# Performance work log

Measured on AMD Instinct MI355X. Metric: run time of the kernel, lower is better.

## Reference

```python
import jax, jax.numpy as jnp
import numpy as np
from jax import lax

B, CIN, COUT, H, W = 8, 128, 128, 128, 128
HID = COUT // 2  # expansion 0.5
K = 3            # kernel size
PAD = 1


def silu(v):
    return v * jax.nn.sigmoid(v)


def base_conv1x1(x, w, s, b):
    # 1x1 conv (no bias) + folded-BN affine (scale s, bias b) + SiLU
    y = jnp.einsum('bchw,oc->bohw', x, w)
    return silu(y * s[None, :, None, None] + b[None, :, None, None])


def bilinear_gather(img, py, px):
    Hin, Win = img.shape[1], img.shape[2]
    y0 = jnp.floor(py)
    x0 = jnp.floor(px)
    wy = py - y0
    wx = px - x0

    def corner(yc, xc):
        valid = (yc >= 0) & (yc <= Hin - 1) & (xc >= 0) & (xc <= Win - 1)
        yi = jnp.clip(yc, 0, Hin - 1).astype(jnp.int32)
        xi = jnp.clip(xc, 0, Win - 1).astype(jnp.int32)
        v = img[:, yi, xi]  # [C, Kk, H, W]
        return v * valid[None].astype(img.dtype)

    v00 = corner(y0, x0)
    v01 = corner(y0, x0 + 1)
    v10 = corner(y0 + 1, x0)
    v11 = corner(y0 + 1, x0 + 1)
    wy = wy[None]
    wx = wx[None]
    return (v00 * (1 - wy) * (1 - wx) + v01 * (1 - wy) * wx
            + v10 * wy * (1 - wx) + v11 * wy * wx)


def deform_conv_depthwise(x, off_w, off_b, dw):
    # x: [B, C, H, W]; off_w: [2*K*K, C, 3, 3]; dw: [C, K, K] (depthwise, groups=C)
    b, c, h, w = x.shape
    off = lax.conv_general_dilated(
        x, off_w, window_strides=(1, 1), padding=((PAD, PAD), (PAD, PAD)),
        dimension_numbers=('NCHW', 'OIHW', 'NCHW'))
    off = off + off_b[None, :, None, None]
    off = off.reshape(b, K * K, 2, h, w)  # torchvision: (dy, dx) per tap
    dy, dx = off[:, :, 0], off[:, :, 1]   # [B, 9, H, W]

    ky = jnp.repeat(jnp.arange(K, dtype=x.dtype), K)  # [9]
    kx = jnp.tile(jnp.arange(K, dtype=x.dtype), K)
    yy = jnp.arange(h, dtype=x.dtype)[None, :, None]  # [1, H, 1]
    xx = jnp.arange(w, dtype=x.dtype)[None, None, :]
    py = yy + ky[:, None, None] - PAD  # [9, H, W]
    px = xx + kx[:, None, None] - PAD
    py = py[None] + dy  # [B, 9, H, W]
    px = px[None] + dx

    sampled = jax.vmap(bilinear_gather)(x, py, px)  # [B, C, 9, H, W]
    return jnp.einsum('bckhw,ck->bchw', sampled, dw.reshape(c, K * K))


def setup_inputs() -> dict:
    key = jax.random.key(0)
    ks = jax.random.split(key, 12)
    f = jnp.float32
    inp = {
        'x': jax.random.normal(ks[0], (B, CIN, H, W), f),
        'w1': jax.random.normal(ks[1], (HID, CIN), f) * 0.05,
        's1': jnp.ones((HID,), f), 'b1': jnp.zeros((HID,), f),
        'w2': jax.random.normal(ks[2], (HID, CIN), f) * 0.05,
        's2': jnp.ones((HID,), f), 'b2': jnp.zeros((HID,), f),
        'w3': jax.random.normal(ks[3], (COUT, 2 * HID), f) * 0.05,
        's3': jnp.ones((COUT,), f), 'b3': jnp.zeros((COUT,), f),
        'off_w': jax.random.normal(ks[4], (2 * K * K, HID, K, K), f) * 0.01,
        'off_b': jnp.zeros((2 * K * K,), f),
        'dw': jax.random.normal(ks[5], (HID, K, K), f) * 0.1,
    }
    return inp


def reference(x, w1, s1, b1, w2, s2, b2, w3, s3, b3, off_w, off_b, dw):
    x1 = base_conv1x1(x, w1, s1, b1)          # [B, HID, H, W]
    x2 = base_conv1x1(x, w2, s2, b2)          # [B, HID, H, W]
    x1 = deform_conv_depthwise(x1, off_w, off_b, dw)
    xc = jnp.concatenate([x1, x2], axis=1)    # [B, 2*HID, H, W]
    return base_conv1x1(xc, w3, s3, b3)       # [B, COUT, H, W]
```

## Files before the change

### kernel.cpp

```cpp
#include <hip/hip_runtime.h>

typedef unsigned short u16;
typedef unsigned int   u32;
typedef unsigned char  u8;

#define BB    8
#define CINC  128
#define HIDC  64
#define COUTC 128
#define HH    128
#define WWD   128
#define HWN   16384
#define NPOS  (BB*HWN)

typedef __attribute__((ext_vector_type(8))) short bf16x8;
typedef __attribute__((ext_vector_type(4))) float f32x4;

__device__ __forceinline__ float b2f(u16 u){
    union { u32 i; float f; } v; v.i = ((u32)u) << 16; return v.f;
}
__device__ __forceinline__ u16 f2b(float f){
    union { float f; u32 i; } v; v.f = f;
    u32 i = v.i;
    i += 0x7fffu + ((i >> 16) & 1u);
    return (u16)(i >> 16);
}
__device__ __forceinline__ float blo(u32 u){
    union { u32 i; float f; } v; v.i = u << 16; return v.f;
}
__device__ __forceinline__ float bhi(u32 u){
    union { u32 i; float f; } v; v.i = u & 0xFFFF0000u; return v.f;
}
__device__ __forceinline__ float silu(float y){
    return y / (1.f + __expf(-y));
}

template<bool ISB>
__device__ __forceinline__ float ldp(const void* p, int i){
    if (ISB) return b2f(((const u16*)p)[i]);
    return ((const float*)p)[i];
}

template<bool ISB>
__device__ __forceinline__ void k0_body(
    const void* w1, const void* s1, const void* b1,
    const void* w2, const void* s2, const void* b2,
    const void* w3, const void* s3, const void* b3,
    const void* offw, const void* offb, const void* dw,
    u16* __restrict__ wbc, u16* __restrict__ wb3,
    float* __restrict__ bfc, float* __restrict__ bf3,
    u16* __restrict__ wA, float* __restrict__ ob32, float* __restrict__ dwfT)
{
    int t = blockIdx.x*256 + threadIdx.x;
    if (t < 8192){
        wbc[t] = f2b(ldp<ISB>(w1,t) * ldp<ISB>(s1,t>>7));
    } else if (t < 16384){
        int u = t - 8192;
        wbc[t] = f2b(ldp<ISB>(w2,u) * ldp<ISB>(s2,u>>7));
    }
    if (t < 16384){
        wb3[t] = f2b(ldp<ISB>(w3,t) * ldp<ISB>(s3,t>>7));
    }
    if (t < 18432){
        int set  = t / 9216, rem = t % 9216;
        int tap  = rem / 1024; int rem2 = rem % 1024;
        int chunk= rem2 >> 9;  int rem3 = rem2 & 511;
        int lane = rem3 >> 3;  int jp   = rem3 & 7;
        int jg   = set*16 + (lane & 15);
        int c    = chunk*32 + (lane>>4)*8 + jp;
        float v  = (jg < 18) ? ldp<ISB>(offw, (jg*HIDC + c)*9 + tap) : 0.f;
        wA[t] = f2b(v);
    }
    if (t < HIDC)  bfc[t]      = ldp<ISB>(b1,t);
    if (t >= HIDC && t < 2*HIDC) bfc[t] = ldp<ISB>(b2,t-HIDC);
    if (t < COUTC) bf3[t] = ldp<ISB>(b3,t);
    if (t < 32)    ob32[t] = (t < 18) ? ldp<ISB>(offb,t) : 0.f;
    if (t < HIDC*9){
        int c = t / 9, k = t % 9;
        dwfT[k*HIDC + c] = ldp<ISB>(dw,t);
    }
}

__global__ __launch_bounds__(256) void k0_prep(
    const void* w1, const void* s1, const void* b1,
    const void* w2, const void* s2, const void* b2,
    const void* w3, const void* s3, const void* b3,
    const void* offw, const void* offb, const void* dw,
    u16* wbc, u16* wb3, float* bfc, float* bf3,
    u16* wA, float* ob32, float* dwfT)
{
    bool isb = (((const u32*)s1)[0] == 0x3F803F80u);
    if (isb) k0_body<true >(w1,s1,b1,w2,s2,b2,w3,s3,b3,offw,offb,dw,wbc,wb3,bfc,bf3,wA,ob32,dwfT);
    else     k0_body<false>(w1,s1,b1,w2,s2,b2,w3,s3,b3,offw,offb,dw,wbc,wb3,bfc,bf3,wA,ob32,dwfT);
}

template<bool ISB>
__device__ __forceinline__ void k1_body(const void* __restrict__ xv,
    const u16* __restrict__ wbc, const float* __restrict__ bfc,
    u16* __restrict__ x1, u16* __restrict__ x2, u8* __restrict__ ldsb)
{
    const int lane = threadIdx.x & 63;
    const int n    = lane & 15;
    const int quad = lane >> 4;
    u8* mylds = ldsb + (threadIdx.x>>6)*4096;
    bf16x8 w[8][4];
    #pragma unroll
    for (int mt = 0; mt < 8; ++mt)
        #pragma unroll
        for (int t = 0; t < 4; ++t)
            w[mt][t] = *(const bf16x8*)(wbc + (mt*16 + n)*CINC + t*32 + quad*8);
    float4 bias[8];
    #pragma unroll
    for (int mt = 0; mt < 8; ++mt)
        bias[mt] = *(const float4*)(bfc + mt*16 + quad*4);

    const int wv = blockIdx.x*4 + (threadIdx.x >> 6);
    const int posbase = wv*16;
    const int bidx = posbase >> 14;
    const int hwb  = posbase & (HWN-1);
    f32x4 acc[8];
    #pragma unroll
    for (int mt = 0; mt < 8; ++mt) acc[mt] = (f32x4){0.f,0.f,0.f,0.f};
    #pragma unroll
    for (int t = 0; t < 4; ++t){
        bf16x8 bfr;
        if (ISB){
            const u16* xb = (const u16*)xv + (size_t)bidx*CINC*HWN + hwb + n;
            #pragma unroll
            for (int j = 0; j < 8; ++j)
                bfr[j] = (short)xb[(size_t)(t*32 + quad*8 + j)*HWN];
        } else {
            const float* xb = (const float*)xv + (size_t)bidx*CINC*HWN + hwb + n;
            #pragma unroll
            for (int j = 0; j < 8; ++j)
                bfr[j] = (short)f2b(xb[(size_t)(t*32 + quad*8 + j)*HWN]);
        }
        #pragma unroll
        for (int mt = 0; mt < 8; ++mt)
            acc[mt] = __builtin_amdgcn_mfma_f32_16x16x32_bf16(w[mt][t], bfr, acc[mt], 0,0,0);
    }
    #pragma unroll
    for (int mt = 0; mt < 8; ++mt){
        u32 lo = (u32)f2b(silu(acc[mt][0]+bias[mt].x)) | ((u32)f2b(silu(acc[mt][1]+bias[mt].y))<<16);
        u32 hi = (u32)f2b(silu(acc[mt][2]+bias[mt].z)) | ((u32)f2b(silu(acc[mt][3]+bias[mt].w))<<16);
        int chb = mt*32 + quad*8;
        int sw  = chb ^ ((n&3)<<5);
        *(uint2*)(mylds + n*256 + sw) = make_uint2(lo,hi);
    }
    #pragma unroll
    for (int i = 0; i < 2; ++i){
        int pp = i*8 + (lane>>3);
        int cb = (lane&7)*16;
        int sw = cb ^ ((pp&3)<<5);
        uint4 v1 = *(const uint4*)(mylds + pp*256 + sw);
        uint4 v2 = *(const uint4*)(mylds + pp*256 + 128 + sw);
        *(uint4*)((char*)x1 + (size_t)(posbase+pp)*128 + cb) = v1;
        *(uint4*)((char*)x2 + (size_t)(posbase+pp)*128 + cb) = v2;
    }
}

__global__ __launch_bounds__(256, 2) void k1_mfma(const void* x, const u32* s1probe,
    const u16* wbc, const float* bfc, u16* x1, u16* x2)
{
    __shared__ u8 ldsb[4*4096];
    bool isb = (s1probe[0] == 0x3F803F80u);
    if (isb) k1_body<true >(x, wbc, bfc, x1, x2, ldsb);
    else     k1_body<false>(x, wbc, bfc, x1, x2, ldsb);
}

__global__ __launch_bounds__(256) void k2_mfma(const u16* __restrict__ x1,
    const u16* __restrict__ wA, const float* __restrict__ ob32,
    float* __restrict__ offT)
{
    const int lane = threadIdx.x & 63;
    const int n    = lane & 15;
    const int quad = lane >> 4;
    const int tile = blockIdx.x*4 + (threadIdx.x >> 6);
    const int posbase = tile*16;
    const int b   = posbase >> 14;
    const int hw  = posbase & (HWN-1);
    const int y   = hw >> 7;
    const int x0  = hw & (WWD-1);
    const int xb  = x0 + n - 1;
    const u16* bbase = x1 + (size_t)b*HWN*HIDC;

    f32x4 acc0 = (f32x4){0.f,0.f,0.f,0.f};
    f32x4 acc1 = (f32x4){0.f,0.f,0.f,0.f};

    #pragma unroll
    for (int ky = 0; ky < 3; ++ky){
        int ys = y + ky - 1;
        if ((unsigned)ys >= HH) continue;
        const u16* rowp = bbase + (size_t)ys*WWD*HIDC;
        #pragma unroll
        for (int kx = 0; kx < 3; ++kx){
            int  xs  = xb + kx;
            int  xcl = min(max(xs, 0), WWD-1);
            bool vx  = ((unsigned)xs < WWD);
            const int tap = ky*3 + kx;
            #pragma unroll
            for (int ch = 0; ch < 2; ++ch){
                bf16x8 bfr = *(const bf16x8*)(rowp + xcl*HIDC + ch*32 + quad*8);
                if (!vx) bfr = (bf16x8){0,0,0,0,0,0,0,0};
                bf16x8 a0 = *(const bf16x8*)(wA + ((0*9 + tap)*2 + ch)*512 + lane*8);
                bf16x8 a1 = *(const bf16x8*)(wA + ((1*9 + tap)*2 + ch)*512 + lane*8);
                acc0 = __builtin_amdgcn_mfma_f32_16x16x32_bf16(a0, bfr, acc0, 0,0,0);
                acc1 = __builtin_amdgcn_mfma_f32_16x16x32_bf16(a1, bfr, acc1, 0,0,0);
            }
        }
    }
    #pragma unroll
    for (int r = 0; r < 4; ++r){
        int j0 = quad*4 + r;
        offT[(size_t)j0*NPOS + posbase + n] = acc0[r] + ob32[j0];
        int j1 = 16 + quad*4 + r;
        if (j1 < 18)
            offT[(size_t)j1*NPOS + posbase + n] = acc1[r] + ob32[j1];
    }
}

__global__ __launch_bounds__(256, 2) void k3b_gather(const u16* __restrict__ x1,
    const float* __restrict__ offT, const float* __restrict__ dwfT,
    u16* __restrict__ x1d)
{
    __shared__ float s_dwf[576];
    __shared__ __align__(16) u8 s_meta[16*208];

    const int tid  = threadIdx.x;
    if (tid < 144)
        *(float4*)(s_dwf + tid*4) = *(const float4*)(dwfT + tid*4);

    const int lane = tid & 63;
    const int gw   = blockIdx.x*4 + (tid >> 6);
    const int posw = gw << 2;
    const int p    = lane >> 4;
    const int li   = lane & 15;
    const int pos  = posw + p;
    const int slot = (tid >> 4) * 208;

    if (li < 9){
        const int k = li;
        int hw = pos & (HWN-1);
        int y  = hw >> 7, x = hw & (WWD-1);
        float dy = offT[(size_t)(2*k  )*NPOS + pos];
        float dx = offT[(size_t)(2*k+1)*NPOS + pos];
        float py = (float)(y + k/3 - 1) + dy;
        float px = (float)(x + k%3 - 1) + dx;
        float fy = floorf(py), fx = floorf(px);
        float wy = py - fy,    wx = px - fx;
        int y0 = (int)fy, x0i = (int)fx;
        float vy0 = ((unsigned)y0      < HH)  ? 1.f : 0.f;
        float vy1 = ((unsigned)(y0+1)  < HH)  ? 1.f : 0.f;
        float vx0 = ((unsigned)x0i     < WWD) ? 1.f : 0.f;
        float vx1 = ((unsigned)(x0i+1) < WWD) ? 1.f : 0.f;
        int yc0 = min(max(y0,   0), HH-1),  yc1 = min(max(y0+1, 0), HH-1);
        int xc0 = min(max(x0i,  0), WWD-1), xc1 = min(max(x0i+1, 0), WWD-1);
        float wy1 = 1.f - wy, wx1 = 1.f - wx;
        float4 w4;
        w4.x = wy1*wx1*vy0*vx0;
        w4.y = wy1*wx *vy0*vx1;
        w4.z = wy *wx1*vy1*vx0;
        w4.w = wy *wx *vy1*vx1;
        int o0 = (yc0*WWD + xc0)*HIDC;
        int sx = (xc1 != xc0) ? 1 : 0;
        int sy = (yc1 != yc0) ? 1 : 0;
        *(int*)   (s_meta + slot + 4*k)       = o0 | (sx<<20) | (sy<<21);
        *(float4*)(s_meta + slot + 48 + 16*k) = w4;
    }
    __syncthreads();

    const int b = posw >> 14;
    const u32* xb32 = (const u32*)(x1 + (size_t)b*HWN*HIDC) + li*2;

    float acc0 = 0.f, acc1 = 0.f, acc2 = 0.f, acc3 = 0.f;
    #pragma unroll
    for (int k = 0; k < 9; ++k){
        const int    pk  = *(const int*)   (s_meta + slot + 4*k);
        const float4 f   = *(const float4*)(s_meta + slot + 48 + 16*k);
        const float4 dwf = *(const float4*)(s_dwf + k*HIDC + li*4);
        const int o0  = (pk & 0xFFFFF) >> 1;
        const int dxs = (pk & (1<<20)) ? (HIDC>>1)       : 0;
        const int dys = (pk & (1<<21)) ? ((WWD*HIDC)>>1) : 0;
        const uint2 q00 = *(const uint2*)(xb32 + o0);
        const uint2 q01 = *(const uint2*)(xb32 + o0 + dxs);
        const uint2 q10 = *(const uint2*)(xb32 + o0 + dys);
        const uint2 q11 = *(const uint2*)(xb32 + o0 + dys + dxs);

        float s0 = blo(q00.x)*f.x + blo(q01.x)*f.y + blo(q10.x)*f.z + blo(q11.x)*f.w;
        float s1 = bhi(q00.x)*f.x + bhi(q01.x)*f.y + bhi(q10.x)*f.z + bhi(q11.x)*f.w;
        float s2 = blo(q00.y)*f.x + blo(q01.y)*f.y + blo(q10.y)*f.z + blo(q11.y)*f.w;
        float s3 = bhi(q00.y)*f.x + bhi(q01.y)*f.y + bhi(q10.y)*f.z + bhi(q11.y)*f.w;
        acc0 += s0*dwf.x;
        acc1 += s1*dwf.y;
        acc2 += s2*dwf.z;
        acc3 += s3*dwf.w;
    }

    const u32 r0 = ((u32)f2b(acc1) << 16) | (u32)f2b(acc0);
    const u32 r1 = ((u32)f2b(acc3) << 16) | (u32)f2b(acc2);
    uint2* outp = (uint2*)((u32*)x1d + (size_t)pos*(HIDC/2) + li*2);
    *outp = make_uint2(r0, r1);
}

template<bool ISB>
__device__ __forceinline__ void k4_body(const u16* __restrict__ x1d,
    const u16* __restrict__ x2,
    const u16* __restrict__ wb3, const float* __restrict__ bf3,
    void* __restrict__ out)
{
    const int lane = threadIdx.x & 63;
    const int n    = lane & 15;
    const int quad = lane >> 4;
    bf16x8 w[8][4];
    #pragma unroll
    for (int mt = 0; mt < 8; ++mt)
        #pragma unroll
        for (int t = 0; t < 4; ++t)
            w[mt][t] = *(const bf16x8*)(wb3 + (mt*16 + n)*CINC + t*32 + quad*8);
    float4 bias[8];
    #pragma unroll
    for (int mt = 0; mt < 8; ++mt)
        bias[mt] = *(const float4*)(bf3 + mt*16 + quad*4);

    const int wv = blockIdx.x*4 + (threadIdx.x >> 6);
    const int posbase = wv*16;
    const int bidx = posbase >> 14;
    const int hwb  = posbase & (HWN-1);
    f32x4 acc[8];
    #pragma unroll
    for (int mt = 0; mt < 8; ++mt) acc[mt] = (f32x4){0.f,0.f,0.f,0.f};
    const size_t rowb = (size_t)(posbase + n)*HIDC;
    #pragma unroll
    for (int t = 0; t < 4; ++t){
        const u16* src = (t < 2) ? x1d : x2;
        bf16x8 bfr = *(const bf16x8*)(src + rowb + (t&1)*32 + quad*8);
        #pragma unroll
        for (int mt = 0; mt < 8; ++mt)
            acc[mt] = __builtin_amdgcn_mfma_f32_16x16x32_bf16(w[mt][t], bfr, acc[mt], 0,0,0);
    }
    u16*   ob16 = (u16*)  out + (size_t)bidx*COUTC*HWN + hwb + n;
    float* obf  = (float*)out + (size_t)bidx*COUTC*HWN + hwb + n;
    #pragma unroll
    for (int mt = 0; mt < 8; ++mt){
        #pragma unroll
        for (int r = 0; r < 4; ++r){
            const int o = mt*16 + quad*4 + r;
            const float v = silu(acc[mt][r] + bias[mt][r]);
            if (ISB) ob16[(size_t)o*HWN] = f2b(v);
            else     obf [(size_t)o*HWN] = v;
        }
    }
}

__global__ __launch_bounds__(256, 2) void k4_mfma(const u16* x1d, const u16* x2,
    const u32* s1probe, const u16* wb3, const float* bf3, void* out)
{
    bool isb = (s1probe[0] == 0x3F803F80u);
    if (isb) k4_body<true >(x1d, x2, wb3, bf3, out);
    else     k4_body<false>(x1d, x2, wb3, bf3, out);
}

extern "C" void kernel_launch(void* const* d_in, const int* in_sizes, int n_in,
                              void* d_out, int out_size, void* d_ws, size_t ws_size,
                              hipStream_t stream)
{
    const void* x    = d_in[0];
    const void* w1   = d_in[1];
    const void* s1   = d_in[2];
    const void* b1   = d_in[3];
    const void* w2   = d_in[4];
    const void* s2   = d_in[5];
    const void* b2   = d_in[6];
    const void* w3   = d_in[7];
    const void* s3   = d_in[8];
    const void* b3   = d_in[9];
    const void* offw = d_in[10];
    const void* offb = d_in[11];
    const void* dw   = d_in[12];

    char* ws = (char*)d_ws;
    u16*   x1    = (u16*)  (ws + 0);
    u16*   x2    = (u16*)  (ws + 16777216);
    u16*   x1d   = (u16*)  (ws + 33554432);
    float* offT  = (float*)(ws + 50331648);
    u16*   wbc   = (u16*)  (ws + 59768832);
    u16*   wb3   = (u16*)  (ws + 59801600);
    u16*   wA    = (u16*)  (ws + 59834368);
    float* dwfT  = (float*)(ws + 59871232);
    float* bfc   = (float*)(ws + 59873536);
    float* bf3   = (float*)(ws + 59874048);
    float* ob32  = (float*)(ws + 59874560);

    k0_prep<<<72, 256, 0, stream>>>(w1,s1,b1, w2,s2,b2, w3,s3,b3, offw,offb,dw,
                                    wbc, wb3, bfc, bf3, wA, ob32, dwfT);
    k1_mfma  <<<2048, 256, 0, stream>>>(x, (const u32*)s1, wbc, bfc, x1, x2);
    k2_mfma  <<<2048, 256, 0, stream>>>(x1, wA, ob32, offT);
    k3b_gather<<<NPOS/16, 256, 0, stream>>>(x1, offT, dwfT, x1d);
    k4_mfma  <<<2048, 256, 0, stream>>>(x1d, x2, (const u32*)s1, wb3, bf3, d_out);
}
```

Baseline: 266.9 us.

## Stage input tile in LDS and split output channels across waves in 1x1 convs

The first 1x1 conv kernel now has each block cooperatively load a 64-position by 128-channel input tile with wide vector loads. It packs channel pairs into LDS, so the old strided per-element global gathers go away. Each wave then computes 32 output channels over all 64 positions instead of 128 channels over 16 positions, which cuts per-wave weight registers. The final 1x1 conv uses the same wave/channel split. Outputs are written directly without the LDS transpose, which may make the x1/x2 stores less coalesced.

```diff
diff --git a/kernel.cpp b/kernel.cpp
--- a/kernel.cpp
+++ b/kernel.cpp
@@ -97,75 +97,99 @@
 template<bool ISB>
 __device__ __forceinline__ void k1_body(const void* __restrict__ xv,
     const u16* __restrict__ wbc, const float* __restrict__ bfc,
-    u16* __restrict__ x1, u16* __restrict__ x2, u8* __restrict__ ldsb)
-{
+    u16* __restrict__ x1, u16* __restrict__ x2, u8* __restrict__ sx8)
+{
+    const int posb = blockIdx.x*64;
+    const int bidx = posb >> 14;
+    const int hwb  = posb & (HWN-1);
+
+    {
+        const int R  = threadIdx.x >> 2;
+        const int qq = threadIdx.x & 3;
+        u32* dst = (u32*)(sx8 + R*272 + qq*64);
+        if (ISB){
+            const u16* r0 = (const u16*)xv + (size_t)bidx*CINC*HWN + (size_t)(2*R)*HWN + hwb + qq*16;
+            const u16* r1 = r0 + HWN;
+            uint4 a0 = *(const uint4*)(r0);
+            uint4 a1 = *(const uint4*)(r0 + 8);
+            uint4 c0 = *(const uint4*)(r1);
+            uint4 c1 = *(const uint4*)(r1 + 8);
+            u32 A[8] = {a0.x,a0.y,a0.z,a0.w,a1.x,a1.y,a1.z,a1.w};
+            u32 C[8] = {c0.x,c0.y,c0.z,c0.w,c1.x,c1.y,c1.z,c1.w};
+            #pragma unroll
+            for (int k = 0; k < 8; ++k){
+                dst[2*k]   = (A[k] & 0xFFFFu) | (C[k] << 16);
+                dst[2*k+1] = (A[k] >> 16)     | (C[k] & 0xFFFF0000u);
+            }
+        } else {
+            const float* r0 = (const float*)xv + (size_t)bidx*CINC*HWN + (size_t)(2*R)*HWN + hwb + qq*16;
+            const float* r1 = r0 + HWN;
+            #pragma unroll
+            for (int k = 0; k < 8; ++k){
+                float2 f0 = *(const float2*)(r0 + 2*k);
+                float2 f1 = *(const float2*)(r1 + 2*k);
+                dst[2*k]   = (u32)f2b(f0.x) | ((u32)f2b(f1.x) << 16);
+                dst[2*k+1] = (u32)f2b(f0.y) | ((u32)f2b(f1.y) << 16);
+            }
+        }
+    }
+    __syncthreads();
+
+    const int w    = threadIdx.x >> 6;
     const int lane = threadIdx.x & 63;
     const int n    = lane & 15;
     const int quad = lane >> 4;
-    u8* mylds = ldsb + (threadIdx.x>>6)*4096;
-    bf16x8 w[8][4];
-    #pragma unroll
-    for (int mt = 0; mt < 8; ++mt)
+
+    bf16x8 wf[2][4];
+    #pragma unroll
+    for (int m = 0; m < 2; ++m)
         #pragma unroll
         for (int t = 0; t < 4; ++t)
-            w[mt][t] = *(const bf16x8*)(wbc + (mt*16 + n)*CINC + t*32 + quad*8);
-    float4 bias[8];
-    #pragma unroll
-    for (int mt = 0; mt < 8; ++mt)
-        bias[mt] = *(const float4*)(bfc + mt*16 + quad*4);
-
-    const int wv = blockIdx.x*4 + (threadIdx.x >> 6);
-    const int posbase = wv*16;
-    const int bidx = posbase >> 14;
-    const int hwb  = posbase & (HWN-1);
-    f32x4 acc[8];
-    #pragma unroll
-    for (int mt = 0; mt < 8; ++mt) acc[mt] = (f32x4){0.f,0.f,0.f,0.f};
+            wf[m][t] = *(const bf16x8*)(wbc + (size_t)(w*32 + m*16 + n)*CINC + t*32 + quad*8);
+
+    f32x4 acc[2][4];
+    #pragma unroll
+    for (int m = 0; m < 2; ++m)
+        #pragma unroll
+        for (int s = 0; s < 4; ++s) acc[m][s] = (f32x4){0.f,0.f,0.f,0.f};
+
     #pragma unroll
     for (int t = 0; t < 4; ++t){
-        bf16x8 bfr;
-        if (ISB){
-            const u16* xb = (const u16*)xv + (size_t)bidx*CINC*HWN + hwb + n;
+        #pragma unroll
+        for (int sub = 0; sub < 4; ++sub){
+            union { u32 u[4]; bf16x8 v; } bb;
             #pragma unroll
-            for (int j = 0; j < 8; ++j)
-                bfr[j] = (short)xb[(size_t)(t*32 + quad*8 + j)*HWN];
-        } else {
-            const float* xb = (const float*)xv + (size_t)bidx*CINC*HWN + hwb + n;
-            #pragma unroll
-            for (int j = 0; j < 8; ++j)
-                bfr[j] = (short)f2b(xb[(size_t)(t*32 + quad*8 + j)*HWN]);
-        }
-        #pragma unroll
-        for (int mt = 0; mt < 8; ++mt)
-            acc[mt] = __builtin_amdgcn_mfma_f32_16x16x32_bf16(w[mt][t], bfr, acc[mt], 0,0,0);
-    }
-    #pragma unroll
-    for (int mt = 0; mt < 8; ++mt){
-        u32 lo = (u32)f2b(silu(acc[mt][0]+bias[mt].x)) | ((u32)f2b(silu(acc[mt][1]+bias[mt].y))<<16);
-        u32 hi = (u32)f2b(silu(acc[mt][2]+bias[mt].z)) | ((u32)f2b(silu(acc[mt][3]+bias[mt].w))<<16);
-        int chb = mt*32 + quad*8;
-        int sw  = chb ^ ((n&3)<<5);
-        *(uint2*)(mylds + n*256 + sw) = make_uint2(lo,hi);
-    }
-    #pragma unroll
-    for (int i = 0; i < 2; ++i){
-        int pp = i*8 + (lane>>3);
-        int cb = (lane&7)*16;
-        int sw = cb ^ ((pp&3)<<5);
-        uint4 v1 = *(const uint4*)(mylds + pp*256 + sw);
-        uint4 v2 = *(const uint4*)(mylds + pp*256 + 128 + sw);
-        *(uint4*)((char*)x1 + (size_t)(posbase+pp)*128 + cb) = v1;
-        *(uint4*)((char*)x2 + (size_t)(posbase+pp)*128 + cb) = v2;
-    }
-}
-
-__global__ __launch_bounds__(256, 2) void k1_mfma(const void* x, const u32* s1probe,
+            for (int jp = 0; jp < 4; ++jp)
+                bb.u[jp] = *(const u32*)(sx8 + (t*16 + quad*4 + jp)*272 + (sub*16 + n)*4);
+            acc[0][sub] = __builtin_amdgcn_mfma_f32_16x16x32_bf16(wf[0][t], bb.v, acc[0][sub], 0,0,0);
+            acc[1][sub] = __builtin_amdgcn_mfma_f32_16x16x32_bf16(wf[1][t], bb.v, acc[1][sub], 0,0,0);
+        }
+    }
+
+    #pragma unroll
+    for (int m = 0; m < 2; ++m){
+        const int ob = w*32 + m*16 + quad*4;
+        float4 bi = *(const float4*)(bfc + ob);
+        u16* dbuf = (ob < 64) ? x1 : x2;
+        const int oo = ob & 63;
+        #pragma unroll
+        for (int sub = 0; sub < 4; ++sub){
+            const u32 lo = (u32)f2b(silu(acc[m][sub][0] + bi.x))
+                         | ((u32)f2b(silu(acc[m][sub][1] + bi.y)) << 16);
+            const u32 hi = (u32)f2b(silu(acc[m][sub][2] + bi.z))
+                         | ((u32)f2b(silu(acc[m][sub][3] + bi.w)) << 16);
+            *(uint2*)(dbuf + (size_t)(posb + sub*16 + n)*HIDC + oo) = make_uint2(lo, hi);
+        }
+    }
+}
+
+__global__ __launch_bounds__(256) void k1_mfma(const void* x, const u32* s1probe,
     const u16* wbc, const float* bfc, u16* x1, u16* x2)
 {
-    __shared__ u8 ldsb[4*4096];
+    __shared__ __align__(16) u8 sx8[64*272];
     bool isb = (s1probe[0] == 0x3F803F80u);
-    if (isb) k1_body<true >(x, wbc, bfc, x1, x2, ldsb);
-    else     k1_body<false>(x, wbc, bfc, x1, x2, ldsb);
+    if (isb) k1_body<true >(x, wbc, bfc, x1, x2, sx8);
+    else     k1_body<false>(x, wbc, bfc, x1, x2, sx8);
 }
 
 __global__ __launch_bounds__(256) void k2_mfma(const u16* __restrict__ x1,
@@ -308,51 +332,59 @@
     const u16* __restrict__ wb3, const float* __restrict__ bf3,
     void* __restrict__ out)
 {
+    const int posb = blockIdx.x*64;
+    const int bidx = posb >> 14;
+    const int hwb  = posb & (HWN-1);
+    const int w    = threadIdx.x >> 6;
     const int lane = threadIdx.x & 63;
     const int n    = lane & 15;
     const int quad = lane >> 4;
-    bf16x8 w[8][4];
-    #pragma unroll
-    for (int mt = 0; mt < 8; ++mt)
+
+    bf16x8 wf[2][4];
+    #pragma unroll
+    for (int m = 0; m < 2; ++m)
         #pragma unroll
         for (int t = 0; t < 4; ++t)
-            w[mt][t] = *(const bf16x8*)(wb3 + (mt*16 + n)*CINC + t*32 + quad*8);
-    float4 bias[8];
-    #pragma unroll
-    for (int mt = 0; mt < 8; ++mt)
-        bias[mt] = *(const float4*)(bf3 + mt*16 + quad*4);
-
-    const int wv = blockIdx.x*4 + (threadIdx.x >> 6);
-    const int posbase = wv*16;
-    const int bidx = posbase >> 14;
-    const int hwb  = posbase & (HWN-1);
-    f32x4 acc[8];
-    #pragma unroll
-    for (int mt = 0; mt < 8; ++mt) acc[mt] = (f32x4){0.f,0.f,0.f,0.f};
-    const size_t rowb = (size_t)(posbase + n)*HIDC;
+            wf[m][t] = *(const bf16x8*)(wb3 + (size_t)(w*32 + m*16 + n)*CINC + t*32 + quad*8);
+
+    f32x4 acc[2][4];
+    #pragma unroll
+    for (int m = 0; m < 2; ++m)
+        #pragma unroll
+        for (int s = 0; s < 4; ++s) acc[m][s] = (f32x4){0.f,0.f,0.f,0.f};
+
     #pragma unroll
     for (int t = 0; t < 4; ++t){
         const u16* src = (t < 2) ? x1d : x2;
-        bf16x8 bfr = *(const bf16x8*)(src + rowb + (t&1)*32 + quad*8);
-        #pragma unroll
-        for (int mt = 0; mt < 8; ++mt)
-            acc[mt] = __builtin_amdgcn_mfma_f32_16x16x32_bf16(w[mt][t], bfr, acc[mt], 0,0,0);
-    }
-    u16*   ob16 = (u16*)  out + (size_t)bidx*COUTC*HWN + hwb + n;
-    float* obf  = (float*)out + (size_t)bidx*COUTC*HWN + hwb + n;
-    #pragma unroll
-    for (int mt = 0; mt < 8; ++mt){
-        #pragma unroll
-        for (int r = 0; r < 4; ++r){
-            const int o = mt*16 + quad*4 + r;
-            const float v = silu(acc[mt][r] + bias[mt][r]);
-            if (ISB) ob16[(size_t)o*HWN] = f2b(v);
-            else     obf [(size_t)o*HWN] = v;
-        }
-    }
-}
-
-__global__ __launch_bounds__(256, 2) void k4_mfma(const u16* x1d, const u16* x2,
+        #pragma unroll
+        for (int sub = 0; sub < 4; ++sub){
+            bf16x8 bfr = *(const bf16x8*)(src + (size_t)(posb + sub*16 + n)*HIDC + (t&1)*32 + quad*8);
+            acc[0][sub] = __builtin_amdgcn_mfma_f32_16x16x32_bf16(wf[0][t], bfr, acc[0][sub], 0,0,0);
+            acc[1][sub] = __builtin_amdgcn_mfma_f32_16x16x32_bf16(wf[1][t], bfr, acc[1][sub], 0,0,0);
+        }
+    }
+
+    u16*   ob16 = (u16*)  out + (size_t)bidx*COUTC*HWN + hwb;
+    float* obf  = (float*)out + (size_t)bidx*COUTC*HWN + hwb;
+    #pragma unroll
+    for (int m = 0; m < 2; ++m){
+        const int ob = w*32 + m*16 + quad*4;
+        float4 bi = *(const float4*)(bf3 + ob);
+        #pragma unroll
+        for (int sub = 0; sub < 4; ++sub){
+            const int pp = sub*16 + n;
+            #pragma unroll
+            for (int r = 0; r < 4; ++r){
+                const float bv = (r==0)?bi.x:(r==1)?bi.y:(r==2)?bi.z:bi.w;
+                const float v = silu(acc[m][sub][r] + bv);
+                if (ISB) ob16[(size_t)(ob+r)*HWN + pp] = f2b(v);
+                else     obf [(size_t)(ob+r)*HWN + pp] = v;
+            }
+        }
+    }
+}
+
+__global__ __launch_bounds__(256) void k4_mfma(const u16* x1d, const u16* x2,
     const u32* s1probe, const u16* wb3, const float* bf3, void* out)
 {
     bool isb = (s1probe[0] == 0x3F803F80u);
@@ -393,8 +425,8 @@
 
     k0_prep<<<72, 256, 0, stream>>>(w1,s1,b1, w2,s2,b2, w3,s3,b3, offw,offb,dw,
                                     wbc, wb3, bfc, bf3, wA, ob32, dwfT);
-    k1_mfma  <<<2048, 256, 0, stream>>>(x, (const u32*)s1, wbc, bfc, x1, x2);
+    k1_mfma  <<<NPOS/64, 256, 0, stream>>>(x, (const u32*)s1, wbc, bfc, x1, x2);
     k2_mfma  <<<2048, 256, 0, stream>>>(x1, wA, ob32, offT);
     k3b_gather<<<NPOS/16, 256, 0, stream>>>(x1, offT, dwfT, x1d);
-    k4_mfma  <<<2048, 256, 0, stream>>>(x1d, x2, (const u32*)s1, wb3, bf3, d_out);
-}
+    k4_mfma  <<<NPOS/64, 256, 0, stream>>>(x1d, x2, (const u32*)s1, wb3, bf3, d_out);
+}
```

Result: faster. 242.2 us (-9.3%).
